# Kernel tuning notes

Hardware: AMD Instinct MI355X
Metric: run time of the kernel (lower is better)

## Reference

```python
import jax, jax.numpy as jnp
import numpy as np

B, T = 64, 512
IN, OUT, H = 256, 256, 1024


def _lstm_cell(x, h, c, Wih, Whh, bih, bhh):
    # PyTorch LSTMCell: gates = x@Wih^T + bih + h@Whh^T + bhh, order i,f,g,o
    gates = x @ Wih.T + bih + h @ Whh.T + bhh
    i, f, g, o = jnp.split(gates, 4, axis=-1)
    c_new = jax.nn.sigmoid(f) * c + jax.nn.sigmoid(i) * jnp.tanh(g)
    h_new = jax.nn.sigmoid(o) * jnp.tanh(c_new)
    return h_new, c_new


def setup_inputs() -> dict:
    key = jax.random.key(0)
    ks = jax.random.split(key, 12)
    s = 1.0 / np.sqrt(H)  # torch default uniform(-1/sqrt(H), 1/sqrt(H))
    u = lambda k, shp: jax.random.uniform(k, shp, jnp.float32, -s, s)
    return {
        "z": jax.random.normal(ks[0], (B, H), jnp.float32),
        "x": jax.random.normal(ks[1], (B, T, IN), jnp.float32),
        "Wih0": u(ks[2], (4 * H, IN)),
        "Whh0": u(ks[3], (4 * H, H)),
        "bih0": u(ks[4], (4 * H,)),
        "bhh0": u(ks[5], (4 * H,)),
        "Wih1": u(ks[6], (4 * H, H)),
        "Whh1": u(ks[7], (4 * H, H)),
        "bih1": u(ks[8], (4 * H,)),
        "bhh1": u(ks[9], (4 * H,)),
        "Wlin": u(ks[10], (OUT, H)),
        "blin": u(ks[11], (OUT,)),
    }


def reference(z, x, Wih0, Whh0, bih0, bhh0, Wih1, Whh1, bih1, bhh1, Wlin, blin):
    # Teacher-forcing unroll: h_t[l] init to z, c_t[l] init to 0, first input is zeros,
    # then input at step t+1 is x[:, t].
    x_tb = jnp.swapaxes(x, 0, 1)  # [T, B, IN]
    c0_init = jnp.zeros_like(z)

    def step(carry, x_t):
        cur_in, h0, c0, h1, c1 = carry
        h0, c0 = _lstm_cell(cur_in, h0, c0, Wih0, Whh0, bih0, bhh0)
        h1, c1 = _lstm_cell(h0, h1, c1, Wih1, Whh1, bih1, bhh1)
        out_t = h1 @ Wlin.T + blin  # [B, OUT]
        return (x_t, h0, c0, h1, c1), out_t

    init = (jnp.zeros((z.shape[0], Wih0.shape[1]), z.dtype), z, c0_init, z, c0_init)
    _, outs = jax.lax.scan(step, init, x_tb)  # outs: [T, B, OUT]
    return jnp.swapaxes(outs, 0, 1)  # [B, T, OUT]
```

## Files before the change

kernel.cpp:

```cpp
#include <hip/hip_runtime.h>
#include <hip/hip_bf16.h>
#include <math.h>


typedef __attribute__((ext_vector_type(8))) short bf16x8;
typedef __attribute__((ext_vector_type(4))) float f32x4;
typedef unsigned long long u64;

__device__ __forceinline__ float sigm(float v) {
  return 1.f / (1.f + __expf(-v));
}
__device__ __forceinline__ float ftanh(float v) {
  return 2.f / (1.f + __expf(-2.f * v)) - 1.f;
}

__device__ __forceinline__ unsigned short bf16_bits(float v) {
  __hip_bfloat16 hb = __float2bfloat16(v);
  unsigned short us;
  __builtin_memcpy(&us, &hb, 2);
  return us;
}

__device__ __forceinline__ void vstore_bf16(__hip_bfloat16* p, float v) {
  *(volatile unsigned short*)p = bf16_bits(v);
}


__global__ __launch_bounds__(256) void prep_w0(const float* __restrict__ Wih0,
                                               const float* __restrict__ Whh0,
                                               __hip_bfloat16* __restrict__ W0) {
  const unsigned n = 4096u * 1280u;
  for (unsigned d = blockIdx.x * blockDim.x + threadIdx.x; d < n;
       d += blockDim.x * gridDim.x) {
    unsigned r = d / 1280u;
    unsigned k = d - r * 1280u;
    unsigned u = r >> 2, g = r & 3u;
    unsigned srow = g * 1024u + u;
    float v = (k < 256u) ? Wih0[(size_t)srow * 256u + k]
                         : Whh0[(size_t)srow * 1024u + (k - 256u)];
    W0[d] = __float2bfloat16(v);
  }
}

__global__ __launch_bounds__(256) void prep_w1(const float* __restrict__ Wih1,
                                               const float* __restrict__ Whh1,
                                               const float* __restrict__ Wlin,
                                               __hip_bfloat16* __restrict__ W1) {
  const unsigned n = 4352u * 2048u;
  for (unsigned d = blockIdx.x * blockDim.x + threadIdx.x; d < n;
       d += blockDim.x * gridDim.x) {
    unsigned r = d >> 11;
    unsigned k = d & 2047u;
    float v;
    if (r < 4096u) {
      unsigned u = r >> 2, g = r & 3u;
      unsigned srow = g * 1024u + u;
      v = (k < 1024u) ? Wih1[(size_t)srow * 1024u + k]
                      : Whh1[(size_t)srow * 1024u + (k - 1024u)];
    } else {
      unsigned o = r - 4096u;
      v = (k < 1024u) ? 0.f : Wlin[(size_t)o * 1024u + (k - 1024u)];
    }
    W1[d] = __float2bfloat16(v);
  }
}

__global__ __launch_bounds__(256) void prep_x(const float* __restrict__ x,
                                              __hip_bfloat16* __restrict__ xbf) {
  const unsigned n = 512u * 64u * 256u;
  for (unsigned d = blockIdx.x * blockDim.x + threadIdx.x; d < n;
       d += blockDim.x * gridDim.x) {
    unsigned t = d >> 14;
    unsigned b = (d >> 8) & 63u;
    unsigned k = d & 255u;
    float v = (t == 0u) ? 0.f : x[((size_t)b * 512u + (t - 1u)) * 256u + k];
    xbf[d] = __float2bfloat16(v);
  }
}

__global__ __launch_bounds__(256) void prep_misc(
    const float* __restrict__ bih0, const float* __restrict__ bhh0,
    const float* __restrict__ bih1, const float* __restrict__ bhh1,
    const float* __restrict__ z, float* __restrict__ b0, float* __restrict__ b1,
    __hip_bfloat16* __restrict__ h0buf, __hip_bfloat16* __restrict__ h1buf) {
  for (int i = blockIdx.x * blockDim.x + threadIdx.x; i < 73728;
       i += blockDim.x * gridDim.x) {
    if (i < 4096) {
      int u = i >> 2, g = i & 3;
      b0[i] = bih0[g * 1024 + u] + bhh0[g * 1024 + u];
    } else if (i < 8192) {
      int r = i - 4096;
      int u = r >> 2, g = r & 3;
      b1[r] = bih1[g * 1024 + u] + bhh1[g * 1024 + u];
    } else {
      int j = i - 8192;
      float zv = z[j];
      vstore_bf16(h0buf + j, zv);
      vstore_bf16(h1buf + 2 * 65536 + j, zv);
    }
  }
}


__device__ __forceinline__ void do_proj(const __hip_bfloat16* __restrict__ h1p,
                                        const bf16x8* wp, float (*red)[16][68],
                                        const float* __restrict__ blin,
                                        float* __restrict__ out, int pcol,
                                        int pbat, int t_out, int tid, int w,
                                        int col, int kq) {
  f32x4 a0 = {0.f, 0.f, 0.f, 0.f};
  const __hip_bfloat16* ab =
      h1p + ((size_t)((pbat << 4) + col) << 10) + (w << 7) + (kq << 3);
#pragma unroll
  for (int c = 0; c < 4; ++c) {
    bf16x8 f = *(const bf16x8*)(ab + (c << 5));
    a0 = __builtin_amdgcn_mfma_f32_16x16x32_bf16(f, wp[c], a0, 0, 0, 0);
  }
  *(f32x4*)&red[w][col][(kq << 2)] = a0;
  __syncthreads();
  if (tid < 256) {
    int o_l = tid & 15, b = tid >> 4;
    float v = blin[(pcol << 4) + o_l];
#pragma unroll
    for (int ww = 0; ww < 8; ++ww) v += red[ww][o_l][b];
    out[(((size_t)((pbat << 4) + b) << 9) + (size_t)t_out) * 256 + (pcol << 4) +
        o_l] = v;
  }
}


__global__ __launch_bounds__(512) void k_persist(
    const __hip_bfloat16* __restrict__ xbf, const __hip_bfloat16* __restrict__ W0,
    const __hip_bfloat16* __restrict__ W1, const float* __restrict__ b0,
    const float* __restrict__ b1, const float* __restrict__ blin,
    __hip_bfloat16* __restrict__ h0buf, __hip_bfloat16* __restrict__ h1buf,
    float* __restrict__ out, unsigned* __restrict__ flags) {
  const int tid = threadIdx.x;
  const int lane = tid & 63;
  const int w = tid >> 6;
  const int bid = blockIdx.x;
  const int cb = bid << 4;
  const int col = lane & 15;
  const int kq = lane >> 4;
  const int n = cb + col;
  const bool isproj = (bid >= 64 && bid < 128);
  const int pcol = bid & 15;
  const int pbat = (bid >> 4) & 3;

  __shared__ int s_agg, s_xcd;
  {
    unsigned* lead = flags + 256;
    if (tid == 0) {
      unsigned xcc = 0;
      asm volatile("s_getreg_b32 %0, hwreg(HW_REG_XCC_ID)" : "=s"(xcc));
      xcc &= 7u;
      unsigned old = __hip_atomic_fetch_add(&lead[xcc], 1u, __ATOMIC_RELAXED,
                                            __HIP_MEMORY_SCOPE_AGENT);
      s_agg = (old == 0u) ? 1 : 0;
      s_xcd = (int)xcc;
    }
  }

  bf16x8 wa[5], wb[8], wp[4];
  {
    const __hip_bfloat16* p = W0 + (size_t)n * 1280 + w * 160 + (kq << 3);
#pragma unroll
    for (int c = 0; c < 5; ++c) wa[c] = *(const bf16x8*)(p + (c << 5));
  }
  {
    const __hip_bfloat16* p = W1 + ((size_t)n << 11) + (w << 8) + (kq << 3);
#pragma unroll
    for (int c = 0; c < 8; ++c) wb[c] = *(const bf16x8*)(p + (c << 5));
  }
  if (isproj) {
    const __hip_bfloat16* p = W1 +
        ((size_t)(4096 + (pcol << 4) + col) << 11) + 1024 + (w << 7) + (kq << 3);
#pragma unroll
    for (int c = 0; c < 4; ++c) wp[c] = *(const bf16x8*)(p + (c << 5));
  }

  const int u_l = tid & 3, bq = tid >> 2;
  float bias0[4], bias1[4];
  if (tid < 256) {
#pragma unroll
    for (int g = 0; g < 4; ++g) {
      bias0[g] = b0[cb + (u_l << 2) + g];
      bias1[g] = b1[cb + (u_l << 2) + g];
    }
  }
  float c0v = 0.f, c1v = 0.f;

  __shared__ float red[8][16][68];

  __syncthreads();

  unsigned* rel = flags + 272 + (s_xcd << 4);

  for (int t = 0; t < 512; ++t) {
    const __hip_bfloat16* h0prev = h0buf + ((size_t)(t & 1) << 16);
    const __hip_bfloat16* h0cur = h0buf + ((size_t)((t + 1) & 1) << 16);
    const __hip_bfloat16* h1prev = h1buf + ((size_t)((t + 2) % 3) << 16);

    {
      f32x4 a0 = {0.f, 0.f, 0.f, 0.f}, a1 = a0, a2 = a0, a3 = a0;
#pragma unroll
      for (int c = 0; c < 5; ++c) {
        const int k0 = w * 160 + (c << 5);
        const __hip_bfloat16* ab;
        size_t rs;
        if (k0 < 256) {
          ab = xbf + ((size_t)t << 14) + k0 + (kq << 3);
          rs = 256;
        } else {
          ab = h0prev + (k0 - 256) + (kq << 3);
          rs = 1024;
        }
        bf16x8 f0 = *(const bf16x8*)(ab + (size_t)col * rs);
        bf16x8 f1 = *(const bf16x8*)(ab + (size_t)(16 + col) * rs);
        bf16x8 f2 = *(const bf16x8*)(ab + (size_t)(32 + col) * rs);
        bf16x8 f3 = *(const bf16x8*)(ab + (size_t)(48 + col) * rs);
        a0 = __builtin_amdgcn_mfma_f32_16x16x32_bf16(f0, wa[c], a0, 0, 0, 0);
        a1 = __builtin_amdgcn_mfma_f32_16x16x32_bf16(f1, wa[c], a1, 0, 0, 0);
        a2 = __builtin_amdgcn_mfma_f32_16x16x32_bf16(f2, wa[c], a2, 0, 0, 0);
        a3 = __builtin_amdgcn_mfma_f32_16x16x32_bf16(f3, wa[c], a3, 0, 0, 0);
      }
      *(f32x4*)&red[w][col][(kq << 2)] = a0;
      *(f32x4*)&red[w][col][16 + (kq << 2)] = a1;
      *(f32x4*)&red[w][col][32 + (kq << 2)] = a2;
      *(f32x4*)&red[w][col][48 + (kq << 2)] = a3;
    }
    __syncthreads();
    if (tid < 256) {
      float gg[4];
#pragma unroll
      for (int g = 0; g < 4; ++g) {
        float v = bias0[g];
#pragma unroll
        for (int ww = 0; ww < 8; ++ww) v += red[ww][(u_l << 2) + g][bq];
        gg[g] = v;
      }
      float cn = sigm(gg[1]) * c0v + sigm(gg[0]) * ftanh(gg[2]);
      c0v = cn;
      vstore_bf16((__hip_bfloat16*)h0cur + ((size_t)bq << 10) + (cb >> 2) + u_l,
                  sigm(gg[3]) * ftanh(cn));
    }
    __syncthreads();

    if (isproj && t >= 2) {
      do_proj(h1buf + (((size_t)((t + 1) % 3)) << 16), wp, red, blin, out,
              pcol, pbat, t - 2, tid, w, col, kq);
    } else if (w < 2 && t < 511) {
      const char* px = (const char*)(xbf + ((size_t)(t + 1) << 14));
      const int idx = (w << 6) | lane;
#pragma unroll
      for (int i = 0; i < 4; ++i) {
        unsigned v = *(const unsigned*)(px + ((idx + (i << 7)) << 6));
        asm volatile("" ::"v"(v));
      }
    }

    __builtin_amdgcn_s_waitcnt(0);
    __syncthreads();
    if (tid == 0)
      __hip_atomic_store(&flags[bid], (unsigned)(t + 1), __ATOMIC_RELAXED,
                         __HIP_MEMORY_SCOPE_AGENT);
    if (w == 0) {
      const unsigned tgt = (unsigned)(t + 1);
      if (s_agg) {
        const u64* fq = (const u64*)flags;
        for (;;) {
          u64 q0 = __hip_atomic_load(&fq[2 * lane], __ATOMIC_RELAXED,
                                     __HIP_MEMORY_SCOPE_AGENT);
          u64 q1 = __hip_atomic_load(&fq[2 * lane + 1], __ATOMIC_RELAXED,
                                     __HIP_MEMORY_SCOPE_AGENT);
          int ok = ((unsigned)q0 >= tgt) & ((unsigned)(q0 >> 32) >= tgt) &
                   ((unsigned)q1 >= tgt) & ((unsigned)(q1 >> 32) >= tgt);
          if (__all(ok)) break;
          __builtin_amdgcn_s_sleep(1);
        }
        __builtin_amdgcn_fence(__ATOMIC_ACQUIRE, "agent");
        if (lane == 0)
          __hip_atomic_store(rel, tgt, __ATOMIC_RELAXED,
                             __HIP_MEMORY_SCOPE_AGENT);
      } else {
        while (__hip_atomic_load(rel, __ATOMIC_RELAXED,
                                 __HIP_MEMORY_SCOPE_AGENT) < tgt)
          __builtin_amdgcn_s_sleep(1);
        if (bid < 8) {
          __builtin_amdgcn_fence(__ATOMIC_ACQUIRE, "agent");
        } else {
          __builtin_amdgcn_sched_barrier(0);
          asm volatile("buffer_inv" ::: "memory");
          __builtin_amdgcn_sched_barrier(0);
        }
      }
    }
    __syncthreads();

    {
      const __hip_bfloat16* ab =
          ((w < 4) ? h0cur : h1prev) + ((w & 3) << 8) + (kq << 3);
      f32x4 a0 = {0.f, 0.f, 0.f, 0.f}, a1 = a0, a2 = a0, a3 = a0;
#pragma unroll
      for (int c = 0; c < 8; ++c) {
        const __hip_bfloat16* p = ab + (c << 5);
        bf16x8 f0 = *(const bf16x8*)(p + ((size_t)col << 10));
        bf16x8 f1 = *(const bf16x8*)(p + ((size_t)(16 + col) << 10));
        bf16x8 f2 = *(const bf16x8*)(p + ((size_t)(32 + col) << 10));
        bf16x8 f3 = *(const bf16x8*)(p + ((size_t)(48 + col) << 10));
        a0 = __builtin_amdgcn_mfma_f32_16x16x32_bf16(f0, wb[c], a0, 0, 0, 0);
        a1 = __builtin_amdgcn_mfma_f32_16x16x32_bf16(f1, wb[c], a1, 0, 0, 0);
        a2 = __builtin_amdgcn_mfma_f32_16x16x32_bf16(f2, wb[c], a2, 0, 0, 0);
        a3 = __builtin_amdgcn_mfma_f32_16x16x32_bf16(f3, wb[c], a3, 0, 0, 0);
      }
      *(f32x4*)&red[w][col][(kq << 2)] = a0;
      *(f32x4*)&red[w][col][16 + (kq << 2)] = a1;
      *(f32x4*)&red[w][col][32 + (kq << 2)] = a2;
      *(f32x4*)&red[w][col][48 + (kq << 2)] = a3;
    }
    __syncthreads();
    if (tid < 256) {
      float gg[4];
#pragma unroll
      for (int g = 0; g < 4; ++g) {
        float v = bias1[g];
#pragma unroll
        for (int ww = 0; ww < 8; ++ww) v += red[ww][(u_l << 2) + g][bq];
        gg[g] = v;
      }
      float cn = sigm(gg[1]) * c1v + sigm(gg[0]) * ftanh(gg[2]);
      c1v = cn;
      vstore_bf16(h1buf + ((size_t)(t % 3) << 16) + ((size_t)bq << 10) +
                      (cb >> 2) + u_l,
                  sigm(gg[3]) * ftanh(cn));
    }
    __syncthreads();
  }

  __builtin_amdgcn_s_waitcnt(0);
  __syncthreads();
  if (tid == 0)
    __hip_atomic_store(&flags[bid], 513u, __ATOMIC_RELAXED,
                       __HIP_MEMORY_SCOPE_AGENT);
  if (w == 0 && s_agg) {
    const u64* fq = (const u64*)flags;
    for (;;) {
      u64 q0 = __hip_atomic_load(&fq[2 * lane], __ATOMIC_RELAXED,
                                 __HIP_MEMORY_SCOPE_AGENT);
      u64 q1 = __hip_atomic_load(&fq[2 * lane + 1], __ATOMIC_RELAXED,
                                 __HIP_MEMORY_SCOPE_AGENT);
      int ok = ((unsigned)q0 >= 513u) & ((unsigned)(q0 >> 32) >= 513u) &
               ((unsigned)q1 >= 513u) & ((unsigned)(q1 >> 32) >= 513u);
      if (__all(ok)) break;
      __builtin_amdgcn_s_sleep(1);
    }
    __builtin_amdgcn_fence(__ATOMIC_ACQUIRE, "agent");
    if (lane == 0)
      __hip_atomic_store(rel, 513u, __ATOMIC_RELAXED,
                         __HIP_MEMORY_SCOPE_AGENT);
  }
  if (!isproj) return;
  if (w == 0 && !s_agg) {
    while (__hip_atomic_load(rel, __ATOMIC_RELAXED,
                             __HIP_MEMORY_SCOPE_AGENT) < 513u)
      __builtin_amdgcn_s_sleep(1);
    __builtin_amdgcn_fence(__ATOMIC_ACQUIRE, "agent");
  }
  __syncthreads();
  do_proj(h1buf, wp, red, blin, out, pcol, pbat, 510, tid, w, col, kq);
  __syncthreads();
  do_proj(h1buf + ((size_t)1 << 16), wp, red, blin, out, pcol, pbat, 511, tid,
          w, col, kq);
}


extern "C" void kernel_launch(void* const* d_in, const int* in_sizes, int n_in,
                              void* d_out, int out_size, void* d_ws, size_t ws_size,
                              hipStream_t stream) {
  const float* z = (const float*)d_in[0];
  const float* x = (const float*)d_in[1];
  const float* Wih0 = (const float*)d_in[2];
  const float* Whh0 = (const float*)d_in[3];
  const float* bih0 = (const float*)d_in[4];
  const float* bhh0 = (const float*)d_in[5];
  const float* Wih1 = (const float*)d_in[6];
  const float* Whh1 = (const float*)d_in[7];
  const float* bih1 = (const float*)d_in[8];
  const float* bhh1 = (const float*)d_in[9];
  const float* Wlin = (const float*)d_in[10];
  const float* blin = (const float*)d_in[11];
  float* out = (float*)d_out;

  char* ws = (char*)d_ws;
  __hip_bfloat16* W0 = (__hip_bfloat16*)(ws);
  __hip_bfloat16* W1 = (__hip_bfloat16*)(ws + 10485760);
  __hip_bfloat16* xbf = (__hip_bfloat16*)(ws + 28311552);
  float* b0 = (float*)(ws + 45088768);
  float* b1 = (float*)(ws + 45105152);
  __hip_bfloat16* h0buf = (__hip_bfloat16*)(ws + 45121536);
  __hip_bfloat16* h1buf = (__hip_bfloat16*)(ws + 45383680);
  unsigned* flags = (unsigned*)(ws + 45776896);

  hipMemsetAsync(flags, 0, 4096, stream);
  prep_w0<<<4096, 256, 0, stream>>>(Wih0, Whh0, W0);
  prep_w1<<<4096, 256, 0, stream>>>(Wih1, Whh1, Wlin, W1);
  prep_x<<<4096, 256, 0, stream>>>(x, xbf);
  prep_misc<<<288, 256, 0, stream>>>(bih0, bhh0, bih1, bhh1, z, b0, b1, h0buf,
                                     h1buf);

  k_persist<<<256, 512, 0, stream>>>(xbf, W0, W1, b0, b1, blin, h0buf, h1buf,
                                     out, flags);
}
```

Baseline: 8.848 ms.

## Double waves per block splitting batch halves and move cache invalidation off barrier path

Raises the persistent kernel to 1024 threads per block so each K-slice is handled by two waves that each cover half the batch, halving per-wave MFMA and load work on the recurrent critical path. The acquire fence / buffer_inv is moved from after the grid barrier to before the prefetch/projection phase, and the extra waves prefetch the next x tile. This shortens each wave's serial chain but doubles register pressure and occupancy demand per CU, and relies on the earlier invalidation still being correct for data written by other blocks.

```diff
diff --git a/kernel.cpp b/kernel.cpp
--- a/kernel.cpp
+++ b/kernel.cpp
@@ -108,15 +108,17 @@
                                         float* __restrict__ out, int pcol,
                                         int pbat, int t_out, int tid, int w,
                                         int col, int kq) {
-  f32x4 a0 = {0.f, 0.f, 0.f, 0.f};
-  const __hip_bfloat16* ab =
-      h1p + ((size_t)((pbat << 4) + col) << 10) + (w << 7) + (kq << 3);
-#pragma unroll
-  for (int c = 0; c < 4; ++c) {
-    bf16x8 f = *(const bf16x8*)(ab + (c << 5));
-    a0 = __builtin_amdgcn_mfma_f32_16x16x32_bf16(f, wp[c], a0, 0, 0, 0);
-  }
-  *(f32x4*)&red[w][col][(kq << 2)] = a0;
+  if (w < 8) {
+    f32x4 a0 = {0.f, 0.f, 0.f, 0.f};
+    const __hip_bfloat16* ab =
+        h1p + ((size_t)((pbat << 4) + col) << 10) + (w << 7) + (kq << 3);
+#pragma unroll
+    for (int c = 0; c < 4; ++c) {
+      bf16x8 f = *(const bf16x8*)(ab + (c << 5));
+      a0 = __builtin_amdgcn_mfma_f32_16x16x32_bf16(f, wp[c], a0, 0, 0, 0);
+    }
+    *(f32x4*)&red[w][col][(kq << 2)] = a0;
+  }
   __syncthreads();
   if (tid < 256) {
     int o_l = tid & 15, b = tid >> 4;
@@ -129,7 +131,7 @@
 }
 
 
-__global__ __launch_bounds__(512) void k_persist(
+__global__ __launch_bounds__(1024, 4) void k_persist(
     const __hip_bfloat16* __restrict__ xbf, const __hip_bfloat16* __restrict__ W0,
     const __hip_bfloat16* __restrict__ W1, const float* __restrict__ b0,
     const float* __restrict__ b1, const float* __restrict__ blin,
@@ -138,16 +140,19 @@
   const int tid = threadIdx.x;
   const int lane = tid & 63;
   const int w = tid >> 6;
+  const int ks = w >> 1;
+  const int bh = w & 1;
   const int bid = blockIdx.x;
   const int cb = bid << 4;
   const int col = lane & 15;
   const int kq = lane >> 4;
   const int n = cb + col;
+  const int brow = (bh << 5) + col;
   const bool isproj = (bid >= 64 && bid < 128);
   const int pcol = bid & 15;
   const int pbat = (bid >> 4) & 3;
 
-  __shared__ int s_agg, s_xcd;
+  __shared__ int s_agg, s_lead, s_xcd;
   {
     unsigned* lead = flags + 256;
     if (tid == 0) {
@@ -157,26 +162,30 @@
       unsigned old = __hip_atomic_fetch_add(&lead[xcc], 1u, __ATOMIC_RELAXED,
                                             __HIP_MEMORY_SCOPE_AGENT);
       s_agg = (old == 0u) ? 1 : 0;
+      s_lead = (old == 0u || bid >= 248) ? 1 : 0;
       s_xcd = (int)xcc;
     }
   }
 
   bf16x8 wa[5], wb[8], wp[4];
   {
-    const __hip_bfloat16* p = W0 + (size_t)n * 1280 + w * 160 + (kq << 3);
+    const __hip_bfloat16* p = W0 + (size_t)n * 1280 + ks * 160 + (kq << 3);
 #pragma unroll
     for (int c = 0; c < 5; ++c) wa[c] = *(const bf16x8*)(p + (c << 5));
   }
   {
-    const __hip_bfloat16* p = W1 + ((size_t)n << 11) + (w << 8) + (kq << 3);
+    const __hip_bfloat16* p = W1 + ((size_t)n << 11) + (ks << 8) + (kq << 3);
 #pragma unroll
     for (int c = 0; c < 8; ++c) wb[c] = *(const bf16x8*)(p + (c << 5));
   }
-  if (isproj) {
+  if (isproj && w < 8) {
     const __hip_bfloat16* p = W1 +
         ((size_t)(4096 + (pcol << 4) + col) << 11) + 1024 + (w << 7) + (kq << 3);
 #pragma unroll
     for (int c = 0; c < 4; ++c) wp[c] = *(const bf16x8*)(p + (c << 5));
+  } else {
+#pragma unroll
+    for (int c = 0; c < 4; ++c) wp[c] = bf16x8{0, 0, 0, 0, 0, 0, 0, 0};
   }
 
   const int u_l = tid & 3, bq = tid >> 2;
@@ -202,10 +211,10 @@
     const __hip_bfloat16* h1prev = h1buf + ((size_t)((t + 2) % 3) << 16);
 
     {
-      f32x4 a0 = {0.f, 0.f, 0.f, 0.f}, a1 = a0, a2 = a0, a3 = a0;
+      f32x4 a0 = {0.f, 0.f, 0.f, 0.f}, a1 = a0;
 #pragma unroll
       for (int c = 0; c < 5; ++c) {
-        const int k0 = w * 160 + (c << 5);
+        const int k0 = ks * 160 + (c << 5);
         const __hip_bfloat16* ab;
         size_t rs;
         if (k0 < 256) {
@@ -215,19 +224,13 @@
           ab = h0prev + (k0 - 256) + (kq << 3);
           rs = 1024;
         }
-        bf16x8 f0 = *(const bf16x8*)(ab + (size_t)col * rs);
-        bf16x8 f1 = *(const bf16x8*)(ab + (size_t)(16 + col) * rs);
-        bf16x8 f2 = *(const bf16x8*)(ab + (size_t)(32 + col) * rs);
-        bf16x8 f3 = *(const bf16x8*)(ab + (size_t)(48 + col) * rs);
+        bf16x8 f0 = *(const bf16x8*)(ab + (size_t)brow * rs);
+        bf16x8 f1 = *(const bf16x8*)(ab + (size_t)(16 + brow) * rs);
         a0 = __builtin_amdgcn_mfma_f32_16x16x32_bf16(f0, wa[c], a0, 0, 0, 0);
         a1 = __builtin_amdgcn_mfma_f32_16x16x32_bf16(f1, wa[c], a1, 0, 0, 0);
-        a2 = __builtin_amdgcn_mfma_f32_16x16x32_bf16(f2, wa[c], a2, 0, 0, 0);
-        a3 = __builtin_amdgcn_mfma_f32_16x16x32_bf16(f3, wa[c], a3, 0, 0, 0);
-      }
-      *(f32x4*)&red[w][col][(kq << 2)] = a0;
-      *(f32x4*)&red[w][col][16 + (kq << 2)] = a1;
-      *(f32x4*)&red[w][col][32 + (kq << 2)] = a2;
-      *(f32x4*)&red[w][col][48 + (kq << 2)] = a3;
+      }
+      *(f32x4*)&red[ks][col][(bh << 5) + (kq << 2)] = a0;
+      *(f32x4*)&red[ks][col][(bh << 5) + 16 + (kq << 2)] = a1;
     }
     __syncthreads();
     if (tid < 256) {
@@ -246,17 +249,35 @@
     }
     __syncthreads();
 
+    if (w == 0) {
+      __builtin_amdgcn_sched_barrier(0);
+      if (s_lead) {
+        __builtin_amdgcn_fence(__ATOMIC_ACQUIRE, "agent");
+      } else {
+        asm volatile("buffer_inv" ::: "memory");
+      }
+      __builtin_amdgcn_sched_barrier(0);
+    }
+    __syncthreads();
+
+    if (w >= 8 && t < 511) {
+      const int pks = (w - 8) >> 1, pbh = (w - 8) & 1;
+      const int prow = (pbh << 5) + col;
+      const __hip_bfloat16* xb = xbf + ((size_t)(t + 1) << 14);
+#pragma unroll
+      for (int c = 0; c < 5; ++c) {
+        const int k0 = pks * 160 + (c << 5);
+        if (k0 < 256) {
+          const __hip_bfloat16* abx = xb + k0 + (kq << 3);
+          unsigned v0 = *(const unsigned*)(abx + (size_t)prow * 256);
+          unsigned v1 = *(const unsigned*)(abx + (size_t)(16 + prow) * 256);
+          asm volatile("" ::"v"(v0), "v"(v1));
+        }
+      }
+    }
     if (isproj && t >= 2) {
       do_proj(h1buf + (((size_t)((t + 1) % 3)) << 16), wp, red, blin, out,
               pcol, pbat, t - 2, tid, w, col, kq);
-    } else if (w < 2 && t < 511) {
-      const char* px = (const char*)(xbf + ((size_t)(t + 1) << 14));
-      const int idx = (w << 6) | lane;
-#pragma unroll
-      for (int i = 0; i < 4; ++i) {
-        unsigned v = *(const unsigned*)(px + ((idx + (i << 7)) << 6));
-        asm volatile("" ::"v"(v));
-      }
     }
 
     __builtin_amdgcn_s_waitcnt(0);
@@ -278,7 +299,6 @@
           if (__all(ok)) break;
           __builtin_amdgcn_s_sleep(1);
         }
-        __builtin_amdgcn_fence(__ATOMIC_ACQUIRE, "agent");
         if (lane == 0)
           __hip_atomic_store(rel, tgt, __ATOMIC_RELAXED,
                              __HIP_MEMORY_SCOPE_AGENT);
@@ -286,37 +306,24 @@
         while (__hip_atomic_load(rel, __ATOMIC_RELAXED,
                                  __HIP_MEMORY_SCOPE_AGENT) < tgt)
           __builtin_amdgcn_s_sleep(1);
-        if (bid < 8) {
-          __builtin_amdgcn_fence(__ATOMIC_ACQUIRE, "agent");
-        } else {
-          __builtin_amdgcn_sched_barrier(0);
-          asm volatile("buffer_inv" ::: "memory");
-          __builtin_amdgcn_sched_barrier(0);
-        }
       }
     }
     __syncthreads();
 
     {
       const __hip_bfloat16* ab =
-          ((w < 4) ? h0cur : h1prev) + ((w & 3) << 8) + (kq << 3);
-      f32x4 a0 = {0.f, 0.f, 0.f, 0.f}, a1 = a0, a2 = a0, a3 = a0;
+          ((ks < 4) ? h0cur + (ks << 8) : h1prev + ((ks - 4) << 8)) + (kq << 3);
+      f32x4 a0 = {0.f, 0.f, 0.f, 0.f}, a1 = a0;
 #pragma unroll
       for (int c = 0; c < 8; ++c) {
         const __hip_bfloat16* p = ab + (c << 5);
-        bf16x8 f0 = *(const bf16x8*)(p + ((size_t)col << 10));
-        bf16x8 f1 = *(const bf16x8*)(p + ((size_t)(16 + col) << 10));
-        bf16x8 f2 = *(const bf16x8*)(p + ((size_t)(32 + col) << 10));
-        bf16x8 f3 = *(const bf16x8*)(p + ((size_t)(48 + col) << 10));
+        bf16x8 f0 = *(const bf16x8*)(p + ((size_t)brow << 10));
+        bf16x8 f1 = *(const bf16x8*)(p + ((size_t)(16 + brow) << 10));
         a0 = __builtin_amdgcn_mfma_f32_16x16x32_bf16(f0, wb[c], a0, 0, 0, 0);
         a1 = __builtin_amdgcn_mfma_f32_16x16x32_bf16(f1, wb[c], a1, 0, 0, 0);
-        a2 = __builtin_amdgcn_mfma_f32_16x16x32_bf16(f2, wb[c], a2, 0, 0, 0);
-        a3 = __builtin_amdgcn_mfma_f32_16x16x32_bf16(f3, wb[c], a3, 0, 0, 0);
-      }
-      *(f32x4*)&red[w][col][(kq << 2)] = a0;
-      *(f32x4*)&red[w][col][16 + (kq << 2)] = a1;
-      *(f32x4*)&red[w][col][32 + (kq << 2)] = a2;
-      *(f32x4*)&red[w][col][48 + (kq << 2)] = a3;
+      }
+      *(f32x4*)&red[ks][col][(bh << 5) + (kq << 2)] = a0;
+      *(f32x4*)&red[ks][col][(bh << 5) + 16 + (kq << 2)] = a1;
     }
     __syncthreads();
     if (tid < 256) {
@@ -408,6 +415,6 @@
   prep_misc<<<288, 256, 0, stream>>>(bih0, bhh0, bih1, bhh1, z, b0, b1, h0buf,
                                      h1buf);
 
-  k_persist<<<256, 512, 0, stream>>>(xbf, W0, W1, b0, b1, blin, h0buf, h1buf,
-                                     out, flags);
-}
+  k_persist<<<256, 1024, 0, stream>>>(xbf, W0, W1, b0, b1, blin, h0buf, h1buf,
+                                      out, flags);
+}
```

Result: slower. 10.14 ms (+14.6%).

## Split layers across block groups and pipeline layer0/layer1 with one grid barrier per step

Applied to the files above, without the earlier changes.

Blocks 0-127 now own layer 0 (32 gate columns each) and blocks 128-255 own layer 1, instead of every block computing both layers in sequence. Layer 1 runs one step behind layer 0, so each timestep needs a single grid-wide barrier instead of two serialized phases. Each block keeps twice as many weights in registers, and the projection is folded into the layer-0 half. This raises register pressure and makes the per-step critical path the slower of the two layers.

```diff
diff --git a/kernel.cpp b/kernel.cpp
--- a/kernel.cpp
+++ b/kernel.cpp
@@ -138,11 +138,12 @@
   const int tid = threadIdx.x;
   const int lane = tid & 63;
   const int w = tid >> 6;
+  const int ks = w >> 1;
+  const int ch = w & 1;
   const int bid = blockIdx.x;
-  const int cb = bid << 4;
   const int col = lane & 15;
   const int kq = lane >> 4;
-  const int n = cb + col;
+  const bool isX = (bid < 128);
   const bool isproj = (bid >= 64 && bid < 128);
   const int pcol = bid & 15;
   const int pbat = (bid >> 4) & 3;
@@ -161,111 +162,148 @@
     }
   }
 
-  bf16x8 wa[5], wb[8], wp[4];
+  bf16x8 wa[10], wb[16], wp[4];
+  if (isX) {
+    const int gcol = (bid << 5) + (ch << 4) + col;
+    const __hip_bfloat16* p = W0 + (size_t)gcol * 1280 + ks * 320 + (kq << 3);
+#pragma unroll
+    for (int c = 0; c < 10; ++c) wa[c] = *(const bf16x8*)(p + (c << 5));
+    if (isproj) {
+      const __hip_bfloat16* q = W1 +
+          ((size_t)(4096 + (pcol << 4) + col) << 11) + 1024 + (w << 7) +
+          (kq << 3);
+#pragma unroll
+      for (int c = 0; c < 4; ++c) wp[c] = *(const bf16x8*)(q + (c << 5));
+    } else {
+#pragma unroll
+      for (int c = 0; c < 4; ++c) wp[c] = bf16x8{0, 0, 0, 0, 0, 0, 0, 0};
+    }
+  } else {
+    const int gcol = ((bid - 128) << 5) + (ch << 4) + col;
+    const __hip_bfloat16* p = W1 + ((size_t)gcol << 11) + (ks << 9) + (kq << 3);
+#pragma unroll
+    for (int c = 0; c < 16; ++c) wb[c] = *(const bf16x8*)(p + (c << 5));
+  }
+
+  const int u_l = tid & 7, bq = tid >> 3;
+  const int ubase = (isX ? (bid << 3) : ((bid - 128) << 3));
+  float bias[4];
   {
-    const __hip_bfloat16* p = W0 + (size_t)n * 1280 + w * 160 + (kq << 3);
-#pragma unroll
-    for (int c = 0; c < 5; ++c) wa[c] = *(const bf16x8*)(p + (c << 5));
-  }
-  {
-    const __hip_bfloat16* p = W1 + ((size_t)n << 11) + (w << 8) + (kq << 3);
-#pragma unroll
-    for (int c = 0; c < 8; ++c) wb[c] = *(const bf16x8*)(p + (c << 5));
-  }
-  if (isproj) {
-    const __hip_bfloat16* p = W1 +
-        ((size_t)(4096 + (pcol << 4) + col) << 11) + 1024 + (w << 7) + (kq << 3);
-#pragma unroll
-    for (int c = 0; c < 4; ++c) wp[c] = *(const bf16x8*)(p + (c << 5));
-  }
-
-  const int u_l = tid & 3, bq = tid >> 2;
-  float bias0[4], bias1[4];
-  if (tid < 256) {
-#pragma unroll
-    for (int g = 0; g < 4; ++g) {
-      bias0[g] = b0[cb + (u_l << 2) + g];
-      bias1[g] = b1[cb + (u_l << 2) + g];
-    }
-  }
-  float c0v = 0.f, c1v = 0.f;
-
-  __shared__ float red[8][16][68];
+    const float* bsrc = isX ? b0 : b1;
+#pragma unroll
+    for (int g = 0; g < 4; ++g) bias[g] = bsrc[((ubase + u_l) << 2) + g];
+  }
+  float cv = 0.f;
+
+  __shared__ float red[4][32][68];
 
   __syncthreads();
 
   unsigned* rel = flags + 272 + (s_xcd << 4);
 
-  for (int t = 0; t < 512; ++t) {
-    const __hip_bfloat16* h0prev = h0buf + ((size_t)(t & 1) << 16);
-    const __hip_bfloat16* h0cur = h0buf + ((size_t)((t + 1) & 1) << 16);
-    const __hip_bfloat16* h1prev = h1buf + ((size_t)((t + 2) % 3) << 16);
-
-    {
-      f32x4 a0 = {0.f, 0.f, 0.f, 0.f}, a1 = a0, a2 = a0, a3 = a0;
-#pragma unroll
-      for (int c = 0; c < 5; ++c) {
-        const int k0 = w * 160 + (c << 5);
-        const __hip_bfloat16* ab;
-        size_t rs;
-        if (k0 < 256) {
-          ab = xbf + ((size_t)t << 14) + k0 + (kq << 3);
-          rs = 256;
-        } else {
-          ab = h0prev + (k0 - 256) + (kq << 3);
-          rs = 1024;
-        }
-        bf16x8 f0 = *(const bf16x8*)(ab + (size_t)col * rs);
-        bf16x8 f1 = *(const bf16x8*)(ab + (size_t)(16 + col) * rs);
-        bf16x8 f2 = *(const bf16x8*)(ab + (size_t)(32 + col) * rs);
-        bf16x8 f3 = *(const bf16x8*)(ab + (size_t)(48 + col) * rs);
-        a0 = __builtin_amdgcn_mfma_f32_16x16x32_bf16(f0, wa[c], a0, 0, 0, 0);
-        a1 = __builtin_amdgcn_mfma_f32_16x16x32_bf16(f1, wa[c], a1, 0, 0, 0);
-        a2 = __builtin_amdgcn_mfma_f32_16x16x32_bf16(f2, wa[c], a2, 0, 0, 0);
-        a3 = __builtin_amdgcn_mfma_f32_16x16x32_bf16(f3, wa[c], a3, 0, 0, 0);
+  for (int k = 0; k <= 512; ++k) {
+    if (isX) {
+      if (k < 512) {
+        const __hip_bfloat16* h0prev = h0buf + ((size_t)(k & 1) << 16);
+        f32x4 a0 = {0.f, 0.f, 0.f, 0.f}, a1 = a0, a2 = a0, a3 = a0;
+#pragma unroll
+        for (int c = 0; c < 10; ++c) {
+          const int k0 = ks * 320 + (c << 5);
+          const __hip_bfloat16* ab;
+          size_t rs;
+          if (k0 < 256) {
+            ab = xbf + ((size_t)k << 14) + k0 + (kq << 3);
+            rs = 256;
+          } else {
+            ab = h0prev + (k0 - 256) + (kq << 3);
+            rs = 1024;
+          }
+          bf16x8 f0 = *(const bf16x8*)(ab + (size_t)col * rs);
+          bf16x8 f1 = *(const bf16x8*)(ab + (size_t)(16 + col) * rs);
+          bf16x8 f2 = *(const bf16x8*)(ab + (size_t)(32 + col) * rs);
+          bf16x8 f3 = *(const bf16x8*)(ab + (size_t)(48 + col) * rs);
+          a0 = __builtin_amdgcn_mfma_f32_16x16x32_bf16(f0, wa[c], a0, 0, 0, 0);
+          a1 = __builtin_amdgcn_mfma_f32_16x16x32_bf16(f1, wa[c], a1, 0, 0, 0);
+          a2 = __builtin_amdgcn_mfma_f32_16x16x32_bf16(f2, wa[c], a2, 0, 0, 0);
+          a3 = __builtin_amdgcn_mfma_f32_16x16x32_bf16(f3, wa[c], a3, 0, 0, 0);
+        }
+        const int rc = (ch << 4) + col;
+        *(f32x4*)&red[ks][rc][(kq << 2)] = a0;
+        *(f32x4*)&red[ks][rc][16 + (kq << 2)] = a1;
+        *(f32x4*)&red[ks][rc][32 + (kq << 2)] = a2;
+        *(f32x4*)&red[ks][rc][48 + (kq << 2)] = a3;
+        __syncthreads();
+        {
+          float gg[4];
+#pragma unroll
+          for (int g = 0; g < 4; ++g) {
+            float v = bias[g];
+#pragma unroll
+            for (int ww = 0; ww < 4; ++ww) v += red[ww][(u_l << 2) + g][bq];
+            gg[g] = v;
+          }
+          float cn = sigm(gg[1]) * cv + sigm(gg[0]) * ftanh(gg[2]);
+          cv = cn;
+          vstore_bf16(h0buf + ((size_t)((k + 1) & 1) << 16) +
+                          ((size_t)bq << 10) + ubase + u_l,
+                      sigm(gg[3]) * ftanh(cn));
+        }
+        __syncthreads();
       }
-      *(f32x4*)&red[w][col][(kq << 2)] = a0;
-      *(f32x4*)&red[w][col][16 + (kq << 2)] = a1;
-      *(f32x4*)&red[w][col][32 + (kq << 2)] = a2;
-      *(f32x4*)&red[w][col][48 + (kq << 2)] = a3;
-    }
-    __syncthreads();
-    if (tid < 256) {
-      float gg[4];
-#pragma unroll
-      for (int g = 0; g < 4; ++g) {
-        float v = bias0[g];
-#pragma unroll
-        for (int ww = 0; ww < 8; ++ww) v += red[ww][(u_l << 2) + g][bq];
-        gg[g] = v;
-      }
-      float cn = sigm(gg[1]) * c0v + sigm(gg[0]) * ftanh(gg[2]);
-      c0v = cn;
-      vstore_bf16((__hip_bfloat16*)h0cur + ((size_t)bq << 10) + (cb >> 2) + u_l,
-                  sigm(gg[3]) * ftanh(cn));
-    }
-    __syncthreads();
-
-    if (isproj && t >= 2) {
-      do_proj(h1buf + (((size_t)((t + 1) % 3)) << 16), wp, red, blin, out,
-              pcol, pbat, t - 2, tid, w, col, kq);
-    } else if (w < 2 && t < 511) {
-      const char* px = (const char*)(xbf + ((size_t)(t + 1) << 14));
-      const int idx = (w << 6) | lane;
-#pragma unroll
-      for (int i = 0; i < 4; ++i) {
-        unsigned v = *(const unsigned*)(px + ((idx + (i << 7)) << 6));
-        asm volatile("" ::"v"(v));
+      if (isproj && k >= 3)
+        do_proj(h1buf + (((size_t)(k % 3)) << 16), wp,
+                (float(*)[16][68])red, blin, out, pcol, pbat, k - 3, tid, w,
+                col, kq);
+    } else {
+      if (k >= 1) {
+        const __hip_bfloat16* h0cur = h0buf + ((size_t)(k & 1) << 16);
+        const __hip_bfloat16* h1prev = h1buf + ((size_t)((k + 1) % 3) << 16);
+        f32x4 a0 = {0.f, 0.f, 0.f, 0.f}, a1 = a0, a2 = a0, a3 = a0;
+#pragma unroll
+        for (int c = 0; c < 16; ++c) {
+          const int k0 = (ks << 9) + (c << 5);
+          const __hip_bfloat16* ab =
+              ((k0 < 1024) ? h0cur + k0 : h1prev + (k0 - 1024)) + (kq << 3);
+          bf16x8 f0 = *(const bf16x8*)(ab + ((size_t)col << 10));
+          bf16x8 f1 = *(const bf16x8*)(ab + ((size_t)(16 + col) << 10));
+          bf16x8 f2 = *(const bf16x8*)(ab + ((size_t)(32 + col) << 10));
+          bf16x8 f3 = *(const bf16x8*)(ab + ((size_t)(48 + col) << 10));
+          a0 = __builtin_amdgcn_mfma_f32_16x16x32_bf16(f0, wb[c], a0, 0, 0, 0);
+          a1 = __builtin_amdgcn_mfma_f32_16x16x32_bf16(f1, wb[c], a1, 0, 0, 0);
+          a2 = __builtin_amdgcn_mfma_f32_16x16x32_bf16(f2, wb[c], a2, 0, 0, 0);
+          a3 = __builtin_amdgcn_mfma_f32_16x16x32_bf16(f3, wb[c], a3, 0, 0, 0);
+        }
+        const int rc = (ch << 4) + col;
+        *(f32x4*)&red[ks][rc][(kq << 2)] = a0;
+        *(f32x4*)&red[ks][rc][16 + (kq << 2)] = a1;
+        *(f32x4*)&red[ks][rc][32 + (kq << 2)] = a2;
+        *(f32x4*)&red[ks][rc][48 + (kq << 2)] = a3;
+        __syncthreads();
+        {
+          float gg[4];
+#pragma unroll
+          for (int g = 0; g < 4; ++g) {
+            float v = bias[g];
+#pragma unroll
+            for (int ww = 0; ww < 4; ++ww) v += red[ww][(u_l << 2) + g][bq];
+            gg[g] = v;
+          }
+          float cn = sigm(gg[1]) * cv + sigm(gg[0]) * ftanh(gg[2]);
+          cv = cn;
+          vstore_bf16(h1buf + ((size_t)((k + 2) % 3) << 16) +
+                          ((size_t)bq << 10) + ubase + u_l,
+                      sigm(gg[3]) * ftanh(cn));
+        }
       }
     }
 
     __builtin_amdgcn_s_waitcnt(0);
     __syncthreads();
     if (tid == 0)
-      __hip_atomic_store(&flags[bid], (unsigned)(t + 1), __ATOMIC_RELAXED,
+      __hip_atomic_store(&flags[bid], (unsigned)(k + 1), __ATOMIC_RELAXED,
                          __HIP_MEMORY_SCOPE_AGENT);
     if (w == 0) {
-      const unsigned tgt = (unsigned)(t + 1);
+      const unsigned tgt = (unsigned)(k + 1);
       if (s_agg) {
         const u64* fq = (const u64*)flags;
         for (;;) {
@@ -296,81 +334,15 @@
       }
     }
     __syncthreads();
-
-    {
-      const __hip_bfloat16* ab =
-          ((w < 4) ? h0cur : h1prev) + ((w & 3) << 8) + (kq << 3);
-      f32x4 a0 = {0.f, 0.f, 0.f, 0.f}, a1 = a0, a2 = a0, a3 = a0;
-#pragma unroll
-      for (int c = 0; c < 8; ++c) {
-        const __hip_bfloat16* p = ab + (c << 5);
-        bf16x8 f0 = *(const bf16x8*)(p + ((size_t)col << 10));
-        bf16x8 f1 = *(const bf16x8*)(p + ((size_t)(16 + col) << 10));
-        bf16x8 f2 = *(const bf16x8*)(p + ((size_t)(32 + col) << 10));
-        bf16x8 f3 = *(const bf16x8*)(p + ((size_t)(48 + col) << 10));
-        a0 = __builtin_amdgcn_mfma_f32_16x16x32_bf16(f0, wb[c], a0, 0, 0, 0);
-        a1 = __builtin_amdgcn_mfma_f32_16x16x32_bf16(f1, wb[c], a1, 0, 0, 0);
-        a2 = __builtin_amdgcn_mfma_f32_16x16x32_bf16(f2, wb[c], a2, 0, 0, 0);
-        a3 = __builtin_amdgcn_mfma_f32_16x16x32_bf16(f3, wb[c], a3, 0, 0, 0);
-      }
-      *(f32x4*)&red[w][col][(kq << 2)] = a0;
-      *(f32x4*)&red[w][col][16 + (kq << 2)] = a1;
-      *(f32x4*)&red[w][col][32 + (kq << 2)] = a2;
-      *(f32x4*)&red[w][col][48 + (kq << 2)] = a3;
-    }
+  }
+
+  if (isproj) {
+    do_proj(h1buf, wp, (float(*)[16][68])red, blin, out, pcol, pbat, 510, tid,
+            w, col, kq);
     __syncthreads();
-    if (tid < 256) {
-      float gg[4];
-#pragma unroll
-      for (int g = 0; g < 4; ++g) {
-        float v = bias1[g];
-#pragma unroll
-        for (int ww = 0; ww < 8; ++ww) v += red[ww][(u_l << 2) + g][bq];
-        gg[g] = v;
-      }
-      float cn = sigm(gg[1]) * c1v + sigm(gg[0]) * ftanh(gg[2]);
-      c1v = cn;
-      vstore_bf16(h1buf + ((size_t)(t % 3) << 16) + ((size_t)bq << 10) +
-                      (cb >> 2) + u_l,
-                  sigm(gg[3]) * ftanh(cn));
-    }
-    __syncthreads();
-  }
-
-  __builtin_amdgcn_s_waitcnt(0);
-  __syncthreads();
-  if (tid == 0)
-    __hip_atomic_store(&flags[bid], 513u, __ATOMIC_RELAXED,
-                       __HIP_MEMORY_SCOPE_AGENT);
-  if (w == 0 && s_agg) {
-    const u64* fq = (const u64*)flags;
-    for (;;) {
-      u64 q0 = __hip_atomic_load(&fq[2 * lane], __ATOMIC_RELAXED,
-                                 __HIP_MEMORY_SCOPE_AGENT);
-      u64 q1 = __hip_atomic_load(&fq[2 * lane + 1], __ATOMIC_RELAXED,
-                                 __HIP_MEMORY_SCOPE_AGENT);
-      int ok = ((unsigned)q0 >= 513u) & ((unsigned)(q0 >> 32) >= 513u) &
-               ((unsigned)q1 >= 513u) & ((unsigned)(q1 >> 32) >= 513u);
-      if (__all(ok)) break;
-      __builtin_amdgcn_s_sleep(1);
-    }
-    __builtin_amdgcn_fence(__ATOMIC_ACQUIRE, "agent");
-    if (lane == 0)
-      __hip_atomic_store(rel, 513u, __ATOMIC_RELAXED,
-                         __HIP_MEMORY_SCOPE_AGENT);
-  }
-  if (!isproj) return;
-  if (w == 0 && !s_agg) {
-    while (__hip_atomic_load(rel, __ATOMIC_RELAXED,
-                             __HIP_MEMORY_SCOPE_AGENT) < 513u)
-      __builtin_amdgcn_s_sleep(1);
-    __builtin_amdgcn_fence(__ATOMIC_ACQUIRE, "agent");
-  }
-  __syncthreads();
-  do_proj(h1buf, wp, red, blin, out, pcol, pbat, 510, tid, w, col, kq);
-  __syncthreads();
-  do_proj(h1buf + ((size_t)1 << 16), wp, red, blin, out, pcol, pbat, 511, tid,
-          w, col, kq);
+    do_proj(h1buf + ((size_t)1 << 16), wp, (float(*)[16][68])red, blin, out,
+            pcol, pbat, 511, tid, w, col, kq);
+  }
 }
 
 
```

After: 9.242 ms. 4.5% more time.
